# Kernel optimization log

Measured on AMD Instinct MI355X. Metric: run time of the kernel, lower is better.

## Reference

```python
import jax, jax.numpy as jnp
import numpy as np
import math

D, H, DK, F, V, L = 512, 8, 64, 2048, 8192, 2
B, S, T = 16, 128, 128
EPS = 1e-5


def _ln(x, g, b):
    mu = jnp.mean(x, -1, keepdims=True)
    var = jnp.mean((x - mu) ** 2, -1, keepdims=True)
    return g * (x - mu) * jax.lax.rsqrt(var + EPS) + b


def _pe(length):
    pos = jnp.arange(length, dtype=jnp.float32)[:, None]
    div = jnp.exp(jnp.arange(0, D, 2, dtype=jnp.float32) * (-math.log(10000.0) / D))
    ang = pos * div
    pe = jnp.zeros((length, D), jnp.float32)
    return pe.at[:, 0::2].set(jnp.sin(ang)).at[:, 1::2].set(jnp.cos(ang))


def _attn(q, k, v, src, dst, num_dst):
    # per-edge score = exp(clip((k_src . q_dst)/sqrt(d_k), -5, 5))  [E, H]
    score = jnp.einsum('ehd,ehd->eh', k[src], q[dst]) / math.sqrt(DK)
    score = jnp.exp(jnp.clip(score, -5.0, 5.0))
    wv = jax.ops.segment_sum(v[src] * score[..., None], dst, num_segments=num_dst)
    z = jax.ops.segment_sum(score, dst, num_segments=num_dst)
    return (wv / z[..., None]).reshape(num_dst, D)


def _forward(src_tokens, tgt_tokens, ee_src, ee_dst, dd_src, dd_dst, ed_src, ed_dst, P):
    (src_emb, tgt_emb, eW, eB, elg, elb, eW1, eb1, eW2, eb2, eng, enb,
     dsW, dsB, dcW, dcB, dlg, dlb, dW1, db1, dW2, db2, dng, dnb, gW, gb) = P
    pe = _pe(max(S, T))
    Ne, Nd = B * S, B * T
    xe = (src_emb[src_tokens] * math.sqrt(D) + pe[None, :S]).reshape(Ne, D)
    xd = (tgt_emb[tgt_tokens] * math.sqrt(D) + pe[None, :T]).reshape(Nd, D)
    # encoder stack
    for i in range(L):
        nx = _ln(xe, elg[i, 0], elb[i, 0])
        q = (nx @ eW[i, 0] + eB[i, 0]).reshape(Ne, H, DK)
        k = (nx @ eW[i, 1] + eB[i, 1]).reshape(Ne, H, DK)
        v = (nx @ eW[i, 2] + eB[i, 2]).reshape(Ne, H, DK)
        xe = xe + _attn(q, k, v, ee_src, ee_dst, Ne) @ eW[i, 3] + eB[i, 3]
        nx = _ln(xe, elg[i, 1], elb[i, 1])
        xe = xe + jax.nn.relu(nx @ eW1[i] + eb1[i]) @ eW2[i] + eb2[i]
        if i == L - 1:
            xe = _ln(xe, eng, enb)
    # decoder stack
    for i in range(L):
        nx = _ln(xd, dlg[i, 0], dlb[i, 0])
        q = (nx @ dsW[i, 0] + dsB[i, 0]).reshape(Nd, H, DK)
        k = (nx @ dsW[i, 1] + dsB[i, 1]).reshape(Nd, H, DK)
        v = (nx @ dsW[i, 2] + dsB[i, 2]).reshape(Nd, H, DK)
        xd = xd + _attn(q, k, v, dd_src, dd_dst, Nd) @ dsW[i, 3] + dsB[i, 3]
        nq = _ln(xd, dlg[i, 1], dlb[i, 1])
        nkv = _ln(xe, dlg[i, 1], dlb[i, 1])
        q = (nq @ dcW[i, 0] + dcB[i, 0]).reshape(Nd, H, DK)
        k = (nkv @ dcW[i, 1] + dcB[i, 1]).reshape(Ne, H, DK)
        v = (nkv @ dcW[i, 2] + dcB[i, 2]).reshape(Ne, H, DK)
        xd = xd + _attn(q, k, v, ed_src, ed_dst, Nd) @ dcW[i, 3] + dcB[i, 3]
        nx = _ln(xd, dlg[i, 2], dlb[i, 2])
        xd = xd + jax.nn.relu(nx @ dW1[i] + db1[i]) @ dW2[i] + db2[i]
        if i == L - 1:
            xd = _ln(xd, dng, dnb)
    return jax.nn.log_softmax(xd @ gW + gb, axis=-1)  # [Nd, V]


def setup_inputs() -> dict:
    key = jax.random.key(0)
    ks = iter(jax.random.split(key, 40))
    def nrm(shape, scale=0.02):
        return jax.random.normal(next(ks), shape, dtype=jnp.float32) * scale
    src_tokens = jax.random.randint(next(ks), (B, S), 0, V, dtype=jnp.int32)
    tgt_tokens = jax.random.randint(next(ks), (B, T), 0, V, dtype=jnp.int32)
    # graph structure (per-sentence blocks)
    si, di = np.meshgrid(np.arange(S), np.arange(S), indexing='ij')
    si, di = si.ravel(), di.ravel()
    base = (np.arange(B) * S)[:, None]
    ee_src = (base + si[None, :]).ravel().astype(np.int32)
    ee_dst = (base + di[None, :]).ravel().astype(np.int32)
    m = si <= di  # causal: src pos <= dst pos
    dd_src = (base + si[m][None, :]).ravel().astype(np.int32)
    dd_dst = (base + di[m][None, :]).ravel().astype(np.int32)
    ed_src = ee_src.copy()
    ed_dst = ee_dst.copy()
    inp = dict(
        src_tokens=src_tokens, tgt_tokens=tgt_tokens,
        ee_src=jnp.asarray(ee_src), ee_dst=jnp.asarray(ee_dst),
        dd_src=jnp.asarray(dd_src), dd_dst=jnp.asarray(dd_dst),
        ed_src=jnp.asarray(ed_src), ed_dst=jnp.asarray(ed_dst),
        src_emb=nrm((V, D), 1.0 / math.sqrt(D)), tgt_emb=nrm((V, D), 1.0 / math.sqrt(D)),
        enc_attn_W=nrm((L, 4, D, D)), enc_attn_b=jnp.zeros((L, 4, D), jnp.float32),
        enc_ln_g=jnp.ones((L, 2, D), jnp.float32), enc_ln_b=jnp.zeros((L, 2, D), jnp.float32),
        enc_ff_W1=nrm((L, D, F)), enc_ff_b1=jnp.zeros((L, F), jnp.float32),
        enc_ff_W2=nrm((L, F, D)), enc_ff_b2=jnp.zeros((L, D), jnp.float32),
        enc_norm_g=jnp.ones((D,), jnp.float32), enc_norm_b=jnp.zeros((D,), jnp.float32),
        dec_self_W=nrm((L, 4, D, D)), dec_self_b=jnp.zeros((L, 4, D), jnp.float32),
        dec_cross_W=nrm((L, 4, D, D)), dec_cross_b=jnp.zeros((L, 4, D), jnp.float32),
        dec_ln_g=jnp.ones((L, 3, D), jnp.float32), dec_ln_b=jnp.zeros((L, 3, D), jnp.float32),
        dec_ff_W1=nrm((L, D, F)), dec_ff_b1=jnp.zeros((L, F), jnp.float32),
        dec_ff_W2=nrm((L, F, D)), dec_ff_b2=jnp.zeros((L, D), jnp.float32),
        dec_norm_g=jnp.ones((D,), jnp.float32), dec_norm_b=jnp.zeros((D,), jnp.float32),
        gen_W=nrm((D, V)), gen_b=jnp.zeros((V,), jnp.float32),
    )
    return inp


def reference(src_tokens, tgt_tokens, ee_src, ee_dst, dd_src, dd_dst, ed_src, ed_dst,
              src_emb, tgt_emb, enc_attn_W, enc_attn_b, enc_ln_g, enc_ln_b,
              enc_ff_W1, enc_ff_b1, enc_ff_W2, enc_ff_b2, enc_norm_g, enc_norm_b,
              dec_self_W, dec_self_b, dec_cross_W, dec_cross_b, dec_ln_g, dec_ln_b,
              dec_ff_W1, dec_ff_b1, dec_ff_W2, dec_ff_b2, dec_norm_g, dec_norm_b,
              gen_W, gen_b):
    P = (src_emb, tgt_emb, enc_attn_W, enc_attn_b, enc_ln_g, enc_ln_b,
         enc_ff_W1, enc_ff_b1, enc_ff_W2, enc_ff_b2, enc_norm_g, enc_norm_b,
         dec_self_W, dec_self_b, dec_cross_W, dec_cross_b, dec_ln_g, dec_ln_b,
         dec_ff_W1, dec_ff_b1, dec_ff_W2, dec_ff_b2, dec_norm_g, dec_norm_b, gen_W, gen_b)
    return _forward(src_tokens, tgt_tokens, ee_src, ee_dst, dd_src, dd_dst, ed_src, ed_dst, P)
```

## Files before the change

kernel.cpp:

```cpp
#include <hip/hip_runtime.h>

typedef __attribute__((ext_vector_type(8))) short bfx8;
typedef __attribute__((ext_vector_type(4))) float fx4;

static __device__ __forceinline__ unsigned short f2bf(float f) {
    union { float f; unsigned int u; } v; v.f = f;
    unsigned int i = v.u;
    return (unsigned short)((i + 0x7FFFu + ((i >> 16) & 1u)) >> 16);
}
static __device__ __forceinline__ float bf2f(unsigned short u) {
    union { unsigned int ui; float f; } cv;
    cv.ui = ((unsigned int)u) << 16;
    return cv.f;
}

static __device__ __forceinline__ void gl2lds16(const unsigned short* g, unsigned short* l) {
    unsigned long long gu = (unsigned long long)g;
    unsigned int lu = (unsigned int)(unsigned long long)l;
    __builtin_amdgcn_global_load_lds(
        (const __attribute__((address_space(1))) void*)gu,
        (__attribute__((address_space(3))) void*)lu,
        16, 0, 0);
}

struct TrGroup {
    const float* src;
    unsigned short* dst;
    int srcRowStride;
    int dstRowStride;
    long srcSliceOff;
    long dstSliceOff;
};
struct TrTable {
    TrGroup g[18];
    int zStart[19];
};

__global__ __launch_bounds__(256) void trall_kernel(TrTable tt)
{
    __shared__ unsigned short tile[32][33];
    int z = blockIdx.z;
    int gi = 0;
#pragma unroll 1
    while (z >= tt.zStart[gi + 1]) ++gi;
    int zi = z - tt.zStart[gi];
    const float* s = tt.g[gi].src + (size_t)zi * tt.g[gi].srcSliceOff;
    unsigned short* d = tt.g[gi].dst + (size_t)zi * tt.g[gi].dstSliceOff;
    int srs = tt.g[gi].srcRowStride, drs = tt.g[gi].dstRowStride;
    int n0 = blockIdx.x * 32, k0 = blockIdx.y * 32;
    int tx = threadIdx.x & 31, ty = threadIdx.x >> 5;
#pragma unroll
    for (int i = 0; i < 32; i += 8)
        tile[ty + i][tx] = f2bf(s[(size_t)(k0 + ty + i) * srs + (n0 + tx)]);
    __syncthreads();
#pragma unroll
    for (int i = 0; i < 32; i += 8)
        d[(size_t)(n0 + ty + i) * drs + (k0 + tx)] = tile[tx][ty + i];
}

__global__ __launch_bounds__(256) void embedln_kernel(
    const int* __restrict__ tokA, const int* __restrict__ tokB,
    const float* __restrict__ embA, const float* __restrict__ embB,
    float* __restrict__ outA, float* __restrict__ outB,
    const float* __restrict__ gA, const float* __restrict__ bA,
    const float* __restrict__ gB, const float* __restrict__ bB,
    unsigned short* __restrict__ nxA, unsigned short* __restrict__ nxB)
{
    __shared__ float red[4];
    int idx = blockIdx.x;
    int row = idx & 2047;
    bool e = idx < 2048;
    const int* tok = e ? tokA : tokB;
    const float* emb = e ? embA : embB;
    float* out = e ? outA : outB;
    const float* g = e ? gA : gB;
    const float* bb = e ? bA : bB;
    unsigned short* nx = e ? nxA : nxB;
    int pos = row & 127;
    int t = tok[row];
    int d0 = threadIdx.x, d1 = threadIdx.x + 256;
    auto pe = [&](int d) {
        float ang = (float)pos * expf((float)(d & ~1) * (-9.210340371976184f / 512.0f));
        return (d & 1) ? cosf(ang) : sinf(ang);
    };
    float v0 = emb[(size_t)t * 512 + d0] * 22.627416997969522f + pe(d0);
    float v1 = emb[(size_t)t * 512 + d1] * 22.627416997969522f + pe(d1);
    out[(size_t)row * 512 + d0] = v0;
    out[(size_t)row * 512 + d1] = v1;
    int lane = threadIdx.x & 63, wv = threadIdx.x >> 6;
    float s = v0 + v1;
#pragma unroll
    for (int off = 32; off; off >>= 1) s += __shfl_xor(s, off);
    if (lane == 0) red[wv] = s;
    __syncthreads();
    float mu = (red[0] + red[1] + red[2] + red[3]) * (1.0f / 512.0f);
    __syncthreads();
    float q = (v0 - mu) * (v0 - mu) + (v1 - mu) * (v1 - mu);
#pragma unroll
    for (int off = 32; off; off >>= 1) q += __shfl_xor(q, off);
    if (lane == 0) red[wv] = q;
    __syncthreads();
    float rs = rsqrtf((red[0] + red[1] + red[2] + red[3]) * (1.0f / 512.0f) + 1e-5f);
    nx[(size_t)row * 512 + d0] = f2bf(g[d0] * (v0 - mu) * rs + bb[d0]);
    nx[(size_t)row * 512 + d1] = f2bf(g[d1] * (v1 - mu) * rs + bb[d1]);
}

static __device__ __forceinline__ void ln_row(
    const float* __restrict__ xrow, const float* __restrict__ g,
    const float* __restrict__ b, int lane, fx4& o0, fx4& o1)
{
    const fx4* xr = (const fx4*)xrow;
    fx4 a = xr[lane * 2], c = xr[lane * 2 + 1];
    float s = a[0] + a[1] + a[2] + a[3] + c[0] + c[1] + c[2] + c[3];
#pragma unroll
    for (int off = 32; off; off >>= 1) s += __shfl_xor(s, off);
    float mu = s * (1.0f / 512.0f);
    float qv = 0.f;
#pragma unroll
    for (int j = 0; j < 4; ++j) {
        float d0 = a[j] - mu; qv += d0 * d0;
        float d1 = c[j] - mu; qv += d1 * d1;
    }
#pragma unroll
    for (int off = 32; off; off >>= 1) qv += __shfl_xor(qv, off);
    float rs = rsqrtf(qv * (1.0f / 512.0f) + 1e-5f);
    const fx4* gr = (const fx4*)g;
    const fx4* br = (const fx4*)b;
    fx4 g0 = gr[lane * 2], g1 = gr[lane * 2 + 1];
    fx4 b0 = br[lane * 2], b1 = br[lane * 2 + 1];
#pragma unroll
    for (int j = 0; j < 4; ++j) {
        o0[j] = g0[j] * (a[j] - mu) * rs + b0[j];
        o1[j] = g1[j] * (c[j] - mu) * rs + b1[j];
    }
}

template<bool OUTBF>
__global__ __launch_bounds__(256) void ln_kernel(
    const float* __restrict__ x, const float* __restrict__ g,
    const float* __restrict__ b, void* __restrict__ out)
{
    int row = blockIdx.x * 4 + (threadIdx.x >> 6);
    int lane = threadIdx.x & 63;
    fx4 o0, o1;
    ln_row(x + (size_t)row * 512, g, b, lane, o0, o1);
    if (OUTBF) {
        unsigned short* orow = (unsigned short*)out + (size_t)row * 512 + lane * 8;
        ushort4 u0 = {f2bf(o0[0]), f2bf(o0[1]), f2bf(o0[2]), f2bf(o0[3])};
        ushort4 u1 = {f2bf(o1[0]), f2bf(o1[1]), f2bf(o1[2]), f2bf(o1[3])};
        *(ushort4*)orow = u0;
        *(ushort4*)(orow + 4) = u1;
    } else {
        fx4* orow = (fx4*)out + (size_t)row * 128;
        orow[lane * 2] = o0;
        orow[lane * 2 + 1] = o1;
    }
}

__global__ __launch_bounds__(256) void ln3_kernel(
    float* __restrict__ xe, const float* __restrict__ eg, const float* __restrict__ eb,
    const float* __restrict__ g0, const float* __restrict__ b0,
    const float* __restrict__ g1, const float* __restrict__ b1,
    unsigned short* __restrict__ nk0, unsigned short* __restrict__ nk1)
{
    int row = blockIdx.x * 4 + (threadIdx.x >> 6);
    int lane = threadIdx.x & 63;
    fx4 t0, t1;
    ln_row(xe + (size_t)row * 512, eg, eb, lane, t0, t1);
    fx4* orow = (fx4*)(xe + (size_t)row * 512);
    orow[lane * 2] = t0;
    orow[lane * 2 + 1] = t1;
    float s = t0[0] + t0[1] + t0[2] + t0[3] + t1[0] + t1[1] + t1[2] + t1[3];
#pragma unroll
    for (int off = 32; off; off >>= 1) s += __shfl_xor(s, off);
    float mu = s * (1.0f / 512.0f);
    float q = 0.f;
#pragma unroll
    for (int j = 0; j < 4; ++j) {
        float a = t0[j] - mu; q += a * a;
        float c = t1[j] - mu; q += c * c;
    }
#pragma unroll
    for (int off = 32; off; off >>= 1) q += __shfl_xor(q, off);
    float rs = rsqrtf(q * (1.0f / 512.0f) + 1e-5f);
    const fx4* g0r = (const fx4*)g0; const fx4* b0r = (const fx4*)b0;
    const fx4* g1r = (const fx4*)g1; const fx4* b1r = (const fx4*)b1;
    fx4 ga0 = g0r[lane * 2], ga1 = g0r[lane * 2 + 1];
    fx4 bb0 = b0r[lane * 2], bb1 = b0r[lane * 2 + 1];
    fx4 gc0 = g1r[lane * 2], gc1 = g1r[lane * 2 + 1];
    fx4 bc0 = b1r[lane * 2], bc1 = b1r[lane * 2 + 1];
    unsigned short* o0 = nk0 + (size_t)row * 512 + lane * 8;
    unsigned short* o1 = nk1 + (size_t)row * 512 + lane * 8;
    ushort4 ua0, ua1, uc0, uc1;
#pragma unroll
    for (int j = 0; j < 4; ++j) {
        float n0 = (t0[j] - mu) * rs, n1 = (t1[j] - mu) * rs;
        ((unsigned short*)&ua0)[j] = f2bf(ga0[j] * n0 + bb0[j]);
        ((unsigned short*)&ua1)[j] = f2bf(ga1[j] * n1 + bb1[j]);
        ((unsigned short*)&uc0)[j] = f2bf(gc0[j] * n0 + bc0[j]);
        ((unsigned short*)&uc1)[j] = f2bf(gc1[j] * n1 + bc1[j]);
    }
    *(ushort4*)o0 = ua0; *(ushort4*)(o0 + 4) = ua1;
    *(ushort4*)o1 = uc0; *(ushort4*)(o1 + 4) = uc1;
}

template<bool RELU, bool RESID, bool OUTBF>
__global__ __launch_bounds__(256) void gemm_bk128_kernel(
    const unsigned short* __restrict__ A, const unsigned short* __restrict__ Wt,
    const float* __restrict__ bias, const float* __restrict__ res,
    void* __restrict__ Cv, int K, int ldc, int gx)
{
    __shared__ unsigned short smem[2][2][8192];
    const int tid = threadIdx.x;
    const int nwg = gridDim.x;
    const int cpx = nwg >> 3;
    const int phys = blockIdx.x;
    const int logical = (phys & 7) * cpx + (phys >> 3);
    const int bm = (logical / gx) * 64;
    const int bn = (logical % gx) * 64;
    const int lane = tid & 63;
    const int wv = tid >> 6;
    const int wr = (wv >> 1) * 32;
    const int wc = (wv & 1) * 32;
    const int lr = lane & 15;
    const int lrow4 = lane >> 4;
    const int lchk16 = lane & 15;
    fx4 acc00 = {0.f, 0.f, 0.f, 0.f}, acc01 = {0.f, 0.f, 0.f, 0.f};
    fx4 acc10 = {0.f, 0.f, 0.f, 0.f}, acc11 = {0.f, 0.f, 0.f, 0.f};

    auto stage = [&](int buf, int k0) {
#pragma unroll
        for (int j = 0; j < 4; ++j) {
            int row = wv * 16 + j * 4 + lrow4;
            int sc = (lchk16 ^ (row & 15)) * 8;
            gl2lds16(A + (size_t)(bm + row) * K + k0 + sc,
                     &smem[buf][0][(wv * 16 + j * 4) * 128]);
            gl2lds16(Wt + (size_t)(bn + row) * K + k0 + sc,
                     &smem[buf][1][(wv * 16 + j * 4) * 128]);
        }
    };

    const int nt = K >> 7;
    int cur = 0;
    stage(0, 0);
    for (int t = 0; t < nt; ++t) {
        __syncthreads();
        if (t + 1 < nt) stage(cur ^ 1, (t + 1) << 7);
        const unsigned short* bufA = &smem[cur][0][0];
        const unsigned short* bufB = &smem[cur][1][0];
        const int ra0 = wr + lr, ra1 = wr + 16 + lr;
        const int rb0 = wc + lr, rb1 = wc + 16 + lr;
        __builtin_amdgcn_s_setprio(1);
#pragma unroll
        for (int kk = 0; kk < 4; ++kk) {
            int ca = kk * 4 + (lane >> 4);
            bfx8 a0 = *(const bfx8*)&bufA[ra0 * 128 + ((ca ^ (ra0 & 15)) * 8)];
            bfx8 a1 = *(const bfx8*)&bufA[ra1 * 128 + ((ca ^ (ra1 & 15)) * 8)];
            bfx8 b0 = *(const bfx8*)&bufB[rb0 * 128 + ((ca ^ (rb0 & 15)) * 8)];
            bfx8 b1 = *(const bfx8*)&bufB[rb1 * 128 + ((ca ^ (rb1 & 15)) * 8)];
            acc00 = __builtin_amdgcn_mfma_f32_16x16x32_bf16(a0, b0, acc00, 0, 0, 0);
            acc01 = __builtin_amdgcn_mfma_f32_16x16x32_bf16(a0, b1, acc01, 0, 0, 0);
            acc10 = __builtin_amdgcn_mfma_f32_16x16x32_bf16(a1, b0, acc10, 0, 0, 0);
            acc11 = __builtin_amdgcn_mfma_f32_16x16x32_bf16(a1, b1, acc11, 0, 0, 0);
        }
        __builtin_amdgcn_s_setprio(0);
        cur ^= 1;
    }
    int rbase = bm + wr + ((lane >> 4) * 4);
    int cbase = bn + wc + lr;
#pragma unroll
    for (int m = 0; m < 2; ++m) {
        fx4 am0 = m ? acc10 : acc00;
        fx4 am1 = m ? acc11 : acc01;
#pragma unroll
        for (int r = 0; r < 4; ++r) {
            int row = rbase + m * 16 + r;
#pragma unroll
            for (int half = 0; half < 2; ++half) {
                int col = cbase + half * 16;
                float v = (half ? am1[r] : am0[r]) + bias[col];
                if (RESID) v += res[(size_t)row * ldc + col];
                if (RELU) v = fmaxf(v, 0.f);
                if (OUTBF) ((unsigned short*)Cv)[(size_t)row * ldc + col] = f2bf(v);
                else       ((float*)Cv)[(size_t)row * ldc + col] = v;
            }
        }
    }
}

template<bool RELU>
__global__ __launch_bounds__(256) void gemm128_kernel(
    const unsigned short* __restrict__ A, const unsigned short* __restrict__ Wt,
    const float* __restrict__ bias, unsigned short* __restrict__ C,
    int K, int ldc)
{
    __shared__ unsigned short smem[2][2][8192];
    const int tid = threadIdx.x;
    const int nwg = gridDim.x;
    const int cpx = nwg >> 3;
    const int phys = blockIdx.x;
    const int logical = (phys & 7) * cpx + (phys >> 3);
    const int bm = (logical & 15) * 128;
    const int bn = (logical >> 4) * 128;
    const int lane = tid & 63;
    const int wv = tid >> 6;
    const int wr = (wv >> 1) * 64;
    const int wc = (wv & 1) * 64;
    const int lr = lane & 15;
    const int lrow = lane >> 3;
    const int lchk = lane & 7;
    fx4 acc[4][4];
#pragma unroll
    for (int mi = 0; mi < 4; ++mi)
#pragma unroll
        for (int ni = 0; ni < 4; ++ni) acc[mi][ni] = fx4{0.f, 0.f, 0.f, 0.f};

    auto stage = [&](int buf, int k0) {
#pragma unroll
        for (int j = 0; j < 4; ++j) {
            int row = wv * 32 + j * 8 + lrow;
            int sc = lchk ^ (row & 7);
            gl2lds16(A + (size_t)(bm + row) * K + k0 + sc * 8,
                     &smem[buf][0][(wv * 32 + j * 8) * 64]);
            gl2lds16(Wt + (size_t)(bn + row) * K + k0 + sc * 8,
                     &smem[buf][1][(wv * 32 + j * 8) * 64]);
        }
    };

    const int nt = K >> 6;
    int cur = 0;
    stage(0, 0);
    for (int t = 0; t < nt; ++t) {
        __syncthreads();
        if (t + 1 < nt) stage(cur ^ 1, (t + 1) << 6);
        const unsigned short* bufA = &smem[cur][0][0];
        const unsigned short* bufB = &smem[cur][1][0];
        __builtin_amdgcn_s_setprio(1);
#pragma unroll
        for (int kk = 0; kk < 2; ++kk) {
            int ca = kk * 4 + (lane >> 4);
            bfx8 af[4], bg[4];
#pragma unroll
            for (int i = 0; i < 4; ++i) {
                int ra = wr + i * 16 + lr;
                int rb = wc + i * 16 + lr;
                af[i] = *(const bfx8*)&bufA[ra * 64 + ((ca ^ (ra & 7)) * 8)];
                bg[i] = *(const bfx8*)&bufB[rb * 64 + ((ca ^ (rb & 7)) * 8)];
            }
#pragma unroll
            for (int mi = 0; mi < 4; ++mi)
#pragma unroll
                for (int ni = 0; ni < 4; ++ni)
                    acc[mi][ni] = __builtin_amdgcn_mfma_f32_16x16x32_bf16(af[mi], bg[ni], acc[mi][ni], 0, 0, 0);
        }
        __builtin_amdgcn_s_setprio(0);
        cur ^= 1;
    }
    int rbase = bm + wr + ((lane >> 4) * 4);
    int cbase = bn + wc + lr;
#pragma unroll
    for (int mi = 0; mi < 4; ++mi)
#pragma unroll
        for (int ni = 0; ni < 4; ++ni) {
            int col = cbase + ni * 16;
            float bv = bias[col];
#pragma unroll
            for (int r = 0; r < 4; ++r) {
                int row = rbase + mi * 16 + r;
                float v = acc[mi][ni][r] + bv;
                if (RELU) v = fmaxf(v, 0.f);
                C[(size_t)row * ldc + col] = f2bf(v);
            }
        }
}

template<bool CAUSAL, bool SELF>
__global__ __launch_bounds__(512) void fattn_kernel(
    const unsigned short* __restrict__ xq, const unsigned short* __restrict__ xkv,
    const unsigned short* __restrict__ Wt, const float* __restrict__ bias,
    unsigned short* __restrict__ out)
{
    constexpr int XROWS = SELF ? 128 : 192;
    constexpr int BUFB  = (XROWS + 192) * 64 * 2;
    __shared__ __align__(16) unsigned char lds[2 * BUFB + 9216 + 18432 + 17408 + 512];
    const int blk = blockIdx.x;
    const int half = blk & 1;
    const int h = (blk >> 1) & 7;
    const int b = blk >> 4;
    const int q0 = half * 64;
    const int tid = threadIdx.x;
    const int lane = tid & 63;
    const int wv = tid >> 6;
    const int lr = lane & 15;
    const int hg8 = (lane >> 4) * 8;
    const int rloc = (lane >> 4) * 4;
    const int lrow = lane >> 3;
    const int lchk = lane & 7;

    const unsigned short* gxq = xq + (size_t)(b * 128 + q0) * 512;
    const unsigned short* gkv = xkv + (size_t)(b * 128) * 512;
    const unsigned short* gw  = Wt + (size_t)(h * 64) * 512;

    auto stage = [&](int buf, int k0) {
        unsigned short* dst = (unsigned short*)(lds + buf * BUFB);
        if constexpr (SELF) {
#pragma unroll
            for (int j = 0; j < 5; ++j) {
                int start = wv * 40 + j * 8;
                int row = start + lrow;
                int sc = (lchk ^ (row & 7)) * 8;
                const unsigned short* src;
                if (start < 128) {
                    src = gkv + (size_t)row * 512 + k0 + sc;
                } else {
                    int wr_ = row - 128;
                    src = gw + ((size_t)(wr_ & 63) + (size_t)(wr_ >> 6) * 512) * 512 + k0 + sc;
                }
                gl2lds16(src, dst + start * 64);
            }
        } else {
            unsigned short* dstW = dst + XROWS * 64;
#pragma unroll
            for (int j = 0; j < 3; ++j) {
                int row = wv * 24 + j * 8 + lrow;
                int sc = (lchk ^ (row & 7)) * 8;
                const unsigned short* xs = (row < 64)
                    ? gxq + (size_t)row * 512
                    : gkv + (size_t)(row - 64) * 512;
                gl2lds16(xs + k0 + sc, dst + (wv * 24 + j * 8) * 64);
                const unsigned short* ws = gw + ((size_t)(row & 63) + (size_t)(row >> 6) * 512) * 512;
                gl2lds16(ws + k0 + sc, dstW + (wv * 24 + j * 8) * 64);
            }
        }
    };

    fx4 accQ[4], accK[4], accV[4];
#pragma unroll
    for (int c = 0; c < 4; ++c) {
        accQ[c] = fx4{0.f, 0.f, 0.f, 0.f};
        accK[c] = fx4{0.f, 0.f, 0.f, 0.f};
        accV[c] = fx4{0.f, 0.f, 0.f, 0.f};
    }
    stage(0, 0);
#pragma unroll 1
    for (int t = 0; t < 8; ++t) {
        __syncthreads();
        if (t < 7) stage((t + 1) & 1, (t + 1) * 64);
        const unsigned short* stX = (const unsigned short*)(lds + (t & 1) * BUFB);
        const unsigned short* stW = stX + XROWS * 64;
#pragma unroll
        for (int kk = 0; kk < 2; ++kk) {
            const int ca = kk * 4 + (lane >> 4);
            auto rd = [&](const unsigned short* base, int row) -> bfx8 {
                return *(const bfx8*)(base + row * 64 + ((ca ^ (row & 7)) * 8));
            };
            const int kvbase = SELF ? 0 : 64;
            bfx8 aKV = rd(stX, kvbase + wv * 16 + lr);
            bfx8 aQ = aKV;
            if (wv >= 4) aQ = rd(stX, (SELF ? q0 : 0) + (wv - 4) * 16 + lr);
            __builtin_amdgcn_s_setprio(1);
#pragma unroll
            for (int c = 0; c < 4; ++c) {
                bfx8 bk = rd(stW, 64 + c * 16 + lr);
                accK[c] = __builtin_amdgcn_mfma_f32_16x16x32_bf16(aKV, bk, accK[c], 0, 0, 0);
                bfx8 bv = rd(stW, 128 + c * 16 + lr);
                accV[c] = __builtin_amdgcn_mfma_f32_16x16x32_bf16(aKV, bv, accV[c], 0, 0, 0);
                if (wv >= 4) {
                    bfx8 bq = rd(stW, c * 16 + lr);
                    accQ[c] = __builtin_amdgcn_mfma_f32_16x16x32_bf16(aQ, bq, accQ[c], 0, 0, 0);
                }
            }
            __builtin_amdgcn_s_setprio(0);
        }
    }
    unsigned short* sQ  = (unsigned short*)(lds + 2 * BUFB);
    unsigned short* sK  = (unsigned short*)(lds + 2 * BUFB + 9216);
    unsigned short* sVt = (unsigned short*)(lds + 2 * BUFB + 9216 + 18432);
    float* zp = (float*)(lds + 2 * BUFB + 9216 + 18432 + 17408);
    unsigned short* sP  = (unsigned short*)lds;
#pragma unroll
    for (int c = 0; c < 4; ++c) {
        int col = c * 16 + lr;
        float bk_ = bias[512 + h * 64 + col];
        float bv_ = bias[1024 + h * 64 + col];
#pragma unroll
        for (int r = 0; r < 4; ++r) {
            sK[(wv * 16 + rloc + r) * 72 + col] = f2bf(accK[c][r] + bk_);
            sVt[col * 136 + (wv * 16 + rloc + r)] = f2bf(accV[c][r] + bv_);
        }
        if (wv >= 4) {
            float bq_ = bias[h * 64 + col];
#pragma unroll
            for (int r = 0; r < 4; ++r)
                sQ[((wv - 4) * 16 + rloc + r) * 72 + col] = f2bf(accQ[c][r] + bq_);
        }
    }
    __syncthreads();
    const int qb = wv >> 1;
    const int kh = wv & 1;
    fx4 acc[4];
#pragma unroll
    for (int n = 0; n < 4; ++n) acc[n] = fx4{0.f, 0.f, 0.f, 0.f};
#pragma unroll
    for (int kk = 0; kk < 2; ++kk) {
        bfx8 a = *(const bfx8*)(sQ + (qb * 16 + lr) * 72 + kk * 32 + hg8);
#pragma unroll
        for (int n = 0; n < 4; ++n) {
            bfx8 bb = *(const bfx8*)(sK + ((kh * 4 + n) * 16 + lr) * 72 + kk * 32 + hg8);
            acc[n] = __builtin_amdgcn_mfma_f32_16x16x32_bf16(a, bb, acc[n], 0, 0, 0);
        }
    }
    const int qg = q0 + qb * 16 + rloc;
#pragma unroll
    for (int r = 0; r < 4; ++r) {
        float zs = 0.f;
#pragma unroll
        for (int n = 0; n < 4; ++n) {
            float s = acc[n][r] * 0.125f;
            s = __expf(fminf(fmaxf(s, -5.f), 5.f));
            if (CAUSAL && (kh * 64 + n * 16 + lr) > (qg + r)) s = 0.f;
            zs += s;
            sP[(qb * 16 + rloc + r) * 136 + kh * 64 + n * 16 + lr] = f2bf(s);
        }
#pragma unroll
        for (int off = 8; off; off >>= 1) zs += __shfl_xor(zs, off);
        if (lr == 0) zp[(qb * 2 + kh) * 16 + rloc + r] = zs;
    }
    __syncthreads();
    float zinv[4];
#pragma unroll
    for (int r = 0; r < 4; ++r)
        zinv[r] = 1.f / (zp[(qb * 2 + 0) * 16 + rloc + r] + zp[(qb * 2 + 1) * 16 + rloc + r]);
    const int dh = wv & 1;
    fx4 acc2[2];
    acc2[0] = fx4{0.f, 0.f, 0.f, 0.f};
    acc2[1] = fx4{0.f, 0.f, 0.f, 0.f};
#pragma unroll
    for (int kk = 0; kk < 4; ++kk) {
        bfx8 a = *(const bfx8*)(sP + (qb * 16 + lr) * 136 + kk * 32 + hg8);
#pragma unroll
        for (int dn = 0; dn < 2; ++dn) {
            bfx8 bb = *(const bfx8*)(sVt + (dh * 32 + dn * 16 + lr) * 136 + kk * 32 + hg8);
            acc2[dn] = __builtin_amdgcn_mfma_f32_16x16x32_bf16(a, bb, acc2[dn], 0, 0, 0);
        }
    }
#pragma unroll
    for (int dn = 0; dn < 2; ++dn)
#pragma unroll
        for (int r = 0; r < 4; ++r) {
            size_t row = (size_t)(b * 128 + qg + r);
            out[row * 512 + h * 64 + dh * 32 + dn * 16 + lr] = f2bf(acc2[dn][r] * zinv[r]);
        }
}

__global__ __launch_bounds__(256) void logsoftmax_bf16_kernel(
    const unsigned short* __restrict__ logits, float* __restrict__ out)
{
    __shared__ float red[4];
    int tid = threadIdx.x;
    const bfx8* lrow = (const bfx8*)(logits + (size_t)blockIdx.x * 8192);
    float* orow = out + (size_t)blockIdx.x * 8192;
    float vals[32];
    float mx = -1e30f;
#pragma unroll
    for (int i = 0; i < 4; ++i) {
        bfx8 u = lrow[i * 256 + tid];
#pragma unroll
        for (int j = 0; j < 8; ++j) {
            float f = bf2f((unsigned short)u[j]);
            vals[i * 8 + j] = f;
            mx = fmaxf(mx, f);
        }
    }
#pragma unroll
    for (int off = 32; off; off >>= 1) mx = fmaxf(mx, __shfl_xor(mx, off));
    int wid = tid >> 6;
    if ((tid & 63) == 0) red[wid] = mx;
    __syncthreads();
    mx = fmaxf(fmaxf(red[0], red[1]), fmaxf(red[2], red[3]));
    __syncthreads();
    float sum = 0.f;
#pragma unroll
    for (int i = 0; i < 32; ++i) sum += __expf(vals[i] - mx);
#pragma unroll
    for (int off = 32; off; off >>= 1) sum += __shfl_xor(sum, off);
    if ((tid & 63) == 0) red[wid] = sum;
    __syncthreads();
    sum = red[0] + red[1] + red[2] + red[3];
    float lsub = mx + logf(sum);
#pragma unroll
    for (int i = 0; i < 4; ++i) {
        fx4 o0, o1;
#pragma unroll
        for (int j = 0; j < 4; ++j) {
            o0[j] = vals[i * 8 + j] - lsub;
            o1[j] = vals[i * 8 + 4 + j] - lsub;
        }
        ((fx4*)orow)[(i * 256 + tid) * 2] = o0;
        ((fx4*)orow)[(i * 256 + tid) * 2 + 1] = o1;
    }
}

extern "C" void kernel_launch(void* const* d_in, const int* in_sizes, int n_in,
                              void* d_out, int out_size, void* d_ws, size_t ws_size,
                              hipStream_t stream) {
    (void)in_sizes; (void)n_in; (void)out_size; (void)ws_size;
    const int* src_tokens = (const int*)d_in[0];
    const int* tgt_tokens = (const int*)d_in[1];
    const float* src_emb    = (const float*)d_in[8];
    const float* tgt_emb    = (const float*)d_in[9];
    const float* enc_attn_W = (const float*)d_in[10];
    const float* enc_attn_b = (const float*)d_in[11];
    const float* enc_ln_g   = (const float*)d_in[12];
    const float* enc_ln_b   = (const float*)d_in[13];
    const float* enc_ff_W1  = (const float*)d_in[14];
    const float* enc_ff_b1  = (const float*)d_in[15];
    const float* enc_ff_W2  = (const float*)d_in[16];
    const float* enc_ff_b2  = (const float*)d_in[17];
    const float* enc_norm_g = (const float*)d_in[18];
    const float* enc_norm_b = (const float*)d_in[19];
    const float* dec_self_W = (const float*)d_in[20];
    const float* dec_self_b = (const float*)d_in[21];
    const float* dec_cross_W= (const float*)d_in[22];
    const float* dec_cross_b= (const float*)d_in[23];
    const float* dec_ln_g   = (const float*)d_in[24];
    const float* dec_ln_b   = (const float*)d_in[25];
    const float* dec_ff_W1  = (const float*)d_in[26];
    const float* dec_ff_b1  = (const float*)d_in[27];
    const float* dec_ff_W2  = (const float*)d_in[28];
    const float* dec_ff_b2  = (const float*)d_in[29];
    const float* dec_norm_g = (const float*)d_in[30];
    const float* dec_norm_b = (const float*)d_in[31];
    const float* gen_W      = (const float*)d_in[32];
    const float* gen_b      = (const float*)d_in[33];
    float* dout = (float*)d_out;

    unsigned short* wt = (unsigned short*)d_ws;
    const size_t OFF_ENCQKV = 0;
    const size_t OFF_ENCO   = 1572864;
    const size_t OFF_ENCW1  = 2097152;
    const size_t OFF_ENCW2  = 4194304;
    const size_t OFF_DECSQKV= 6291456;
    const size_t OFF_DECSO  = 7864320;
    const size_t OFF_DECCQKV= 8388608;
    const size_t OFF_DECCO  = 9961472;
    const size_t OFF_DECW1  = 10485760;
    const size_t OFF_DECW2  = 12582912;
    const size_t OFF_GENW   = 14680064;
    const size_t WT_ELEMS   = 18874368;
    float* fb  = (float*)(wt + WT_ELEMS);
    float* xe  = fb;
    float* xd  = fb + 1048576;
    unsigned short* nxb   = (unsigned short*)(fb + 2097152);
    unsigned short* nxd0  = (unsigned short*)(fb + 3145728);
    unsigned short* ffb   = (unsigned short*)(fb + 4194304);
    unsigned short* nkvb0 = (unsigned short*)(fb + 6291456);
    unsigned short* nkvb1 = (unsigned short*)(fb + 6815744);
    unsigned short* attb  = (unsigned short*)(fb + 7340032);
    unsigned short* genin   = (unsigned short*)fb;
    unsigned short* logitsb = (unsigned short*)(fb + 1048576);

    TrTable tt;
    {
        int z = 0, gi = 0;
        auto addg = [&](const float* s, unsigned short* d, int srs, int drs,
                        long so, long dof, int zc) {
            tt.zStart[gi] = z;
            tt.g[gi].src = s; tt.g[gi].dst = d;
            tt.g[gi].srcRowStride = srs; tt.g[gi].dstRowStride = drs;
            tt.g[gi].srcSliceOff = so; tt.g[gi].dstSliceOff = dof;
            ++gi; z += zc;
        };
        addg(enc_attn_W,              wt + OFF_ENCQKV,               512,  512,  262144,    262144, 3);
        addg(enc_attn_W + 4L*262144,  wt + OFF_ENCQKV + 3L*262144,   512,  512,  262144,    262144, 3);
        addg(enc_attn_W + 3L*262144,  wt + OFF_ENCO,                 512,  512,  4L*262144, 262144, 2);
        addg(enc_ff_W1,               wt + OFF_ENCW1,                2048, 512,  512,       262144, 4);
        addg(enc_ff_W1 + 1048576,     wt + OFF_ENCW1 + 1048576,      2048, 512,  512,       262144, 4);
        addg(enc_ff_W2,               wt + OFF_ENCW2,                512,  2048, 262144,    512,    4);
        addg(enc_ff_W2 + 1048576,     wt + OFF_ENCW2 + 1048576,      512,  2048, 262144,    512,    4);
        addg(dec_self_W,              wt + OFF_DECSQKV,              512,  512,  262144,    262144, 3);
        addg(dec_self_W + 4L*262144,  wt + OFF_DECSQKV + 3L*262144,  512,  512,  262144,    262144, 3);
        addg(dec_self_W + 3L*262144,  wt + OFF_DECSO,                512,  512,  4L*262144, 262144, 2);
        addg(dec_cross_W,             wt + OFF_DECCQKV,              512,  512,  262144,    262144, 3);
        addg(dec_cross_W + 4L*262144, wt + OFF_DECCQKV + 3L*262144,  512,  512,  262144,    262144, 3);
        addg(dec_cross_W + 3L*262144, wt + OFF_DECCO,                512,  512,  4L*262144, 262144, 2);
        addg(dec_ff_W1,               wt + OFF_DECW1,                2048, 512,  512,       262144, 4);
        addg(dec_ff_W1 + 1048576,     wt + OFF_DECW1 + 1048576,      2048, 512,  512,       262144, 4);
        addg(dec_ff_W2,               wt + OFF_DECW2,                512,  2048, 262144,    512,    4);
        addg(dec_ff_W2 + 1048576,     wt + OFF_DECW2 + 1048576,      512,  2048, 262144,    512,    4);
        addg(gen_W,                   wt + OFF_GENW,                 8192, 512,  512,       262144, 16);
        tt.zStart[18] = z;
    }
    trall_kernel<<<dim3(16, 16, 72), 256, 0, stream>>>(tt);

    embedln_kernel<<<4096, 256, 0, stream>>>(
        src_tokens, tgt_tokens, src_emb, tgt_emb, xe, xd,
        enc_ln_g, enc_ln_b, dec_ln_g, dec_ln_b, nxb, nxd0);

    auto gemmK = [&](const unsigned short* A, const unsigned short* W, const float* bias,
                     const float* res, void* C, int N, int K, int ldc, bool relu, bool outbf) {
        int gx = N / 64;
        dim3 g(gx * 32);
        if (res)        gemm_bk128_kernel<false, true,  false><<<g, 256, 0, stream>>>(A, W, bias, res, C, K, ldc, gx);
        else if (relu)  gemm_bk128_kernel<true,  false, true ><<<g, 256, 0, stream>>>(A, W, bias, res, C, K, ldc, gx);
        else if (outbf) gemm_bk128_kernel<false, false, true ><<<g, 256, 0, stream>>>(A, W, bias, res, C, K, ldc, gx);
        else            gemm_bk128_kernel<false, false, false><<<g, 256, 0, stream>>>(A, W, bias, res, C, K, ldc, gx);
    };
    auto gemm128 = [&](const unsigned short* A, const unsigned short* W, const float* bias,
                       unsigned short* C, int N, int K, int ldc, bool relu) {
        dim3 g((N / 128) * 16);
        if (relu) gemm128_kernel<true ><<<g, 256, 0, stream>>>(A, W, bias, C, K, ldc);
        else      gemm128_kernel<false><<<g, 256, 0, stream>>>(A, W, bias, C, K, ldc);
    };
    auto lnb = [&](const float* x, const float* g, const float* b, unsigned short* o) {
        ln_kernel<true><<<512, 256, 0, stream>>>(x, g, b, o);
    };

    for (int i = 0; i < 2; ++i) {
        if (i) lnb(xe, enc_ln_g + (size_t)(i * 2) * 512, enc_ln_b + (size_t)(i * 2) * 512, nxb);
        fattn_kernel<false, true><<<256, 512, 0, stream>>>(
            nxb, nxb, wt + OFF_ENCQKV + (size_t)i * 3 * 262144,
            enc_attn_b + (size_t)i * 4 * 512, attb);
        gemmK(attb, wt + OFF_ENCO + (size_t)i * 262144, enc_attn_b + (size_t)i * 4 * 512 + 1536,
              xe, xe, 512, 512, 512, false, false);
        lnb(xe, enc_ln_g + (size_t)(i * 2 + 1) * 512, enc_ln_b + (size_t)(i * 2 + 1) * 512, nxb);
        gemm128(nxb, wt + OFF_ENCW1 + (size_t)i * 1048576, enc_ff_b1 + (size_t)i * 2048,
                ffb, 2048, 512, 2048, true);
        gemmK(ffb, wt + OFF_ENCW2 + (size_t)i * 1048576, enc_ff_b2 + (size_t)i * 512,
              xe, xe, 512, 2048, 512, false, false);
    }
    ln3_kernel<<<512, 256, 0, stream>>>(
        xe, enc_norm_g, enc_norm_b,
        dec_ln_g + 512, dec_ln_b + 512,
        dec_ln_g + 4 * 512, dec_ln_b + 4 * 512,
        nkvb0, nkvb1);

    for (int i = 0; i < 2; ++i) {
        const unsigned short* qsrc = (i == 0) ? nxd0 : nxb;
        if (i) lnb(xd, dec_ln_g + (size_t)(i * 3) * 512, dec_ln_b + (size_t)(i * 3) * 512, nxb);
        fattn_kernel<true, true><<<256, 512, 0, stream>>>(
            qsrc, qsrc, wt + OFF_DECSQKV + (size_t)i * 3 * 262144,
            dec_self_b + (size_t)i * 4 * 512, attb);
        gemmK(attb, wt + OFF_DECSO + (size_t)i * 262144, dec_self_b + (size_t)i * 4 * 512 + 1536,
              xd, xd, 512, 512, 512, false, false);
        lnb(xd, dec_ln_g + (size_t)(i * 3 + 1) * 512, dec_ln_b + (size_t)(i * 3 + 1) * 512, nxb);
        fattn_kernel<false, false><<<256, 512, 0, stream>>>(
            nxb, i ? nkvb1 : nkvb0, wt + OFF_DECCQKV + (size_t)i * 3 * 262144,
            dec_cross_b + (size_t)i * 4 * 512, attb);
        gemmK(attb, wt + OFF_DECCO + (size_t)i * 262144, dec_cross_b + (size_t)i * 4 * 512 + 1536,
              xd, xd, 512, 512, 512, false, false);
        lnb(xd, dec_ln_g + (size_t)(i * 3 + 2) * 512, dec_ln_b + (size_t)(i * 3 + 2) * 512, nxb);
        gemm128(nxb, wt + OFF_DECW1 + (size_t)i * 1048576, dec_ff_b1 + (size_t)i * 2048,
                ffb, 2048, 512, 2048, true);
        gemmK(ffb, wt + OFF_DECW2 + (size_t)i * 1048576, dec_ff_b2 + (size_t)i * 512,
              xd, xd, 512, 2048, 512, false, false);
    }
    lnb(xd, dec_norm_g, dec_norm_b, genin);

    gemm128(genin, wt + OFF_GENW, gen_b, logitsb, 8192, 512, 8192, false);
    logsoftmax_bf16_kernel<<<2048, 256, 0, stream>>>(logitsb, dout);
}
```

Baseline: 330.0 us.

## Merge weight transpose with embedding kernel and retile QKV projection per wave

```diff
diff --git a/kernel.cpp b/kernel.cpp
--- a/kernel.cpp
+++ b/kernel.cpp
@@ -36,29 +36,8 @@
     int zStart[19];
 };
 
-__global__ __launch_bounds__(256) void trall_kernel(TrTable tt)
-{
-    __shared__ unsigned short tile[32][33];
-    int z = blockIdx.z;
-    int gi = 0;
-#pragma unroll 1
-    while (z >= tt.zStart[gi + 1]) ++gi;
-    int zi = z - tt.zStart[gi];
-    const float* s = tt.g[gi].src + (size_t)zi * tt.g[gi].srcSliceOff;
-    unsigned short* d = tt.g[gi].dst + (size_t)zi * tt.g[gi].dstSliceOff;
-    int srs = tt.g[gi].srcRowStride, drs = tt.g[gi].dstRowStride;
-    int n0 = blockIdx.x * 32, k0 = blockIdx.y * 32;
-    int tx = threadIdx.x & 31, ty = threadIdx.x >> 5;
-#pragma unroll
-    for (int i = 0; i < 32; i += 8)
-        tile[ty + i][tx] = f2bf(s[(size_t)(k0 + ty + i) * srs + (n0 + tx)]);
-    __syncthreads();
-#pragma unroll
-    for (int i = 0; i < 32; i += 8)
-        d[(size_t)(n0 + ty + i) * drs + (k0 + tx)] = tile[tx][ty + i];
-}
-
-__global__ __launch_bounds__(256) void embedln_kernel(
+__global__ __launch_bounds__(256) void prep_kernel(
+    TrTable tt,
     const int* __restrict__ tokA, const int* __restrict__ tokB,
     const float* __restrict__ embA, const float* __restrict__ embB,
     float* __restrict__ outA, float* __restrict__ outB,
@@ -66,16 +45,37 @@
     const float* __restrict__ gB, const float* __restrict__ bB,
     unsigned short* __restrict__ nxA, unsigned short* __restrict__ nxB)
 {
+    __shared__ unsigned short tile[32][33];
     __shared__ float red[4];
-    int idx = blockIdx.x;
-    int row = idx & 2047;
-    bool e = idx < 2048;
-    const int* tok = e ? tokA : tokB;
-    const float* emb = e ? embA : embB;
-    float* out = e ? outA : outB;
-    const float* g = e ? gA : gB;
-    const float* bb = e ? bA : bB;
-    unsigned short* nx = e ? nxA : nxB;
+    int z = blockIdx.z;
+    if (z < 72) {
+        int gi = 0;
+#pragma unroll 1
+        while (z >= tt.zStart[gi + 1]) ++gi;
+        int zi = z - tt.zStart[gi];
+        const float* s = tt.g[gi].src + (size_t)zi * tt.g[gi].srcSliceOff;
+        unsigned short* d = tt.g[gi].dst + (size_t)zi * tt.g[gi].dstSliceOff;
+        int srs = tt.g[gi].srcRowStride, drs = tt.g[gi].dstRowStride;
+        int n0 = blockIdx.x * 32, k0 = blockIdx.y * 32;
+        int tx = threadIdx.x & 31, ty = threadIdx.x >> 5;
+#pragma unroll
+        for (int i = 0; i < 32; i += 8)
+            tile[ty + i][tx] = f2bf(s[(size_t)(k0 + ty + i) * srs + (n0 + tx)]);
+        __syncthreads();
+#pragma unroll
+        for (int i = 0; i < 32; i += 8)
+            d[(size_t)(n0 + ty + i) * drs + (k0 + tx)] = tile[tx][ty + i];
+        return;
+    }
+    int e = (z - 72) * 256 + blockIdx.y * 16 + blockIdx.x;
+    int row = e & 2047;
+    bool isA = e < 2048;
+    const int* tok = isA ? tokA : tokB;
+    const float* emb = isA ? embA : embB;
+    float* out = isA ? outA : outB;
+    const float* g = isA ? gA : gB;
+    const float* bb = isA ? bA : bB;
+    unsigned short* nx = isA ? nxA : nxB;
     int pos = row & 127;
     int t = tok[row];
     int d0 = threadIdx.x, d1 = threadIdx.x + 256;
@@ -434,13 +434,16 @@
         }
     };
 
-    fx4 accQ[4], accK[4], accV[4];
-#pragma unroll
-    for (int c = 0; c < 4; ++c) {
-        accQ[c] = fx4{0.f, 0.f, 0.f, 0.f};
-        accK[c] = fx4{0.f, 0.f, 0.f, 0.f};
-        accV[c] = fx4{0.f, 0.f, 0.f, 0.f};
-    }
+    fx4 acc[4][4];
+#pragma unroll
+    for (int i = 0; i < 4; ++i)
+#pragma unroll
+        for (int c = 0; c < 4; ++c) acc[i][c] = fx4{0.f, 0.f, 0.f, 0.f};
+
+    const int arowbase = (wv == 4) ? (SELF ? q0 : 0)
+                                   : (SELF ? 0 : 64) + ((wv & 1) * 64);
+    const int wbase = (wv == 4) ? 0 : (wv < 2 ? 64 : 128);
+
     stage(0, 0);
 #pragma unroll 1
     for (int t = 0; t < 8; ++t) {
@@ -448,29 +451,26 @@
         if (t < 7) stage((t + 1) & 1, (t + 1) * 64);
         const unsigned short* stX = (const unsigned short*)(lds + (t & 1) * BUFB);
         const unsigned short* stW = stX + XROWS * 64;
-#pragma unroll
-        for (int kk = 0; kk < 2; ++kk) {
-            const int ca = kk * 4 + (lane >> 4);
-            auto rd = [&](const unsigned short* base, int row) -> bfx8 {
-                return *(const bfx8*)(base + row * 64 + ((ca ^ (row & 7)) * 8));
-            };
-            const int kvbase = SELF ? 0 : 64;
-            bfx8 aKV = rd(stX, kvbase + wv * 16 + lr);
-            bfx8 aQ = aKV;
-            if (wv >= 4) aQ = rd(stX, (SELF ? q0 : 0) + (wv - 4) * 16 + lr);
-            __builtin_amdgcn_s_setprio(1);
-#pragma unroll
-            for (int c = 0; c < 4; ++c) {
-                bfx8 bk = rd(stW, 64 + c * 16 + lr);
-                accK[c] = __builtin_amdgcn_mfma_f32_16x16x32_bf16(aKV, bk, accK[c], 0, 0, 0);
-                bfx8 bv = rd(stW, 128 + c * 16 + lr);
-                accV[c] = __builtin_amdgcn_mfma_f32_16x16x32_bf16(aKV, bv, accV[c], 0, 0, 0);
-                if (wv >= 4) {
-                    bfx8 bq = rd(stW, c * 16 + lr);
-                    accQ[c] = __builtin_amdgcn_mfma_f32_16x16x32_bf16(aQ, bq, accQ[c], 0, 0, 0);
+        if (wv < 5) {
+#pragma unroll
+            for (int kk = 0; kk < 2; ++kk) {
+                const int ca = kk * 4 + (lane >> 4);
+                auto rd = [&](const unsigned short* base, int row) -> bfx8 {
+                    return *(const bfx8*)(base + row * 64 + ((ca ^ (row & 7)) * 8));
+                };
+                bfx8 af[4];
+#pragma unroll
+                for (int i = 0; i < 4; ++i) af[i] = rd(stX, arowbase + i * 16 + lr);
+                __builtin_amdgcn_s_setprio(1);
+#pragma unroll
+                for (int c = 0; c < 4; ++c) {
+                    bfx8 bf = rd(stW, wbase + c * 16 + lr);
+#pragma unroll
+                    for (int i = 0; i < 4; ++i)
+                        acc[i][c] = __builtin_amdgcn_mfma_f32_16x16x32_bf16(af[i], bf, acc[i][c], 0, 0, 0);
                 }
+                __builtin_amdgcn_s_setprio(0);
             }
-            __builtin_amdgcn_s_setprio(0);
         }
     }
     unsigned short* sQ  = (unsigned short*)(lds + 2 * BUFB);
@@ -478,36 +478,55 @@
     unsigned short* sVt = (unsigned short*)(lds + 2 * BUFB + 9216 + 18432);
     float* zp = (float*)(lds + 2 * BUFB + 9216 + 18432 + 17408);
     unsigned short* sP  = (unsigned short*)lds;
-#pragma unroll
-    for (int c = 0; c < 4; ++c) {
-        int col = c * 16 + lr;
-        float bk_ = bias[512 + h * 64 + col];
-        float bv_ = bias[1024 + h * 64 + col];
-#pragma unroll
-        for (int r = 0; r < 4; ++r) {
-            sK[(wv * 16 + rloc + r) * 72 + col] = f2bf(accK[c][r] + bk_);
-            sVt[col * 136 + (wv * 16 + rloc + r)] = f2bf(accV[c][r] + bv_);
-        }
-        if (wv >= 4) {
+    if (wv == 4) {
+#pragma unroll
+        for (int c = 0; c < 4; ++c) {
+            int col = c * 16 + lr;
             float bq_ = bias[h * 64 + col];
 #pragma unroll
-            for (int r = 0; r < 4; ++r)
-                sQ[((wv - 4) * 16 + rloc + r) * 72 + col] = f2bf(accQ[c][r] + bq_);
+            for (int i = 0; i < 4; ++i)
+#pragma unroll
+                for (int r = 0; r < 4; ++r)
+                    sQ[(i * 16 + rloc + r) * 72 + col] = f2bf(acc[i][c][r] + bq_);
+        }
+    } else if (wv < 2) {
+        int rb = wv * 64;
+#pragma unroll
+        for (int c = 0; c < 4; ++c) {
+            int col = c * 16 + lr;
+            float bk_ = bias[512 + h * 64 + col];
+#pragma unroll
+            for (int i = 0; i < 4; ++i)
+#pragma unroll
+                for (int r = 0; r < 4; ++r)
+                    sK[(rb + i * 16 + rloc + r) * 72 + col] = f2bf(acc[i][c][r] + bk_);
+        }
+    } else if (wv < 4) {
+        int rb = (wv - 2) * 64;
+#pragma unroll
+        for (int c = 0; c < 4; ++c) {
+            int col = c * 16 + lr;
+            float bv_ = bias[1024 + h * 64 + col];
+#pragma unroll
+            for (int i = 0; i < 4; ++i)
+#pragma unroll
+                for (int r = 0; r < 4; ++r)
+                    sVt[col * 136 + (rb + i * 16 + rloc + r)] = f2bf(acc[i][c][r] + bv_);
         }
     }
     __syncthreads();
     const int qb = wv >> 1;
     const int kh = wv & 1;
-    fx4 acc[4];
-#pragma unroll
-    for (int n = 0; n < 4; ++n) acc[n] = fx4{0.f, 0.f, 0.f, 0.f};
+    fx4 sacc[4];
+#pragma unroll
+    for (int n = 0; n < 4; ++n) sacc[n] = fx4{0.f, 0.f, 0.f, 0.f};
 #pragma unroll
     for (int kk = 0; kk < 2; ++kk) {
         bfx8 a = *(const bfx8*)(sQ + (qb * 16 + lr) * 72 + kk * 32 + hg8);
 #pragma unroll
         for (int n = 0; n < 4; ++n) {
             bfx8 bb = *(const bfx8*)(sK + ((kh * 4 + n) * 16 + lr) * 72 + kk * 32 + hg8);
-            acc[n] = __builtin_amdgcn_mfma_f32_16x16x32_bf16(a, bb, acc[n], 0, 0, 0);
+            sacc[n] = __builtin_amdgcn_mfma_f32_16x16x32_bf16(a, bb, sacc[n], 0, 0, 0);
         }
     }
     const int qg = q0 + qb * 16 + rloc;
@@ -516,7 +535,7 @@
         float zs = 0.f;
 #pragma unroll
         for (int n = 0; n < 4; ++n) {
-            float s = acc[n][r] * 0.125f;
+            float s = sacc[n][r] * 0.125f;
             s = __expf(fminf(fmaxf(s, -5.f), 5.f));
             if (CAUSAL && (kh * 64 + n * 16 + lr) > (qg + r)) s = 0.f;
             zs += s;
@@ -691,10 +710,8 @@
         addg(gen_W,                   wt + OFF_GENW,                 8192, 512,  512,       262144, 16);
         tt.zStart[18] = z;
     }
-    trall_kernel<<<dim3(16, 16, 72), 256, 0, stream>>>(tt);
-
-    embedln_kernel<<<4096, 256, 0, stream>>>(
-        src_tokens, tgt_tokens, src_emb, tgt_emb, xe, xd,
+    prep_kernel<<<dim3(16, 16, 88), 256, 0, stream>>>(
+        tt, src_tokens, tgt_tokens, src_emb, tgt_emb, xe, xd,
         enc_ln_g, enc_ln_b, dec_ln_g, dec_ln_b, nxb, nxd0);
 
     auto gemmK = [&](const unsigned short* A, const unsigned short* W, const float* bias,
```

After: 307.1 us. 1.07x faster.
